# Kernel tuning notes

Hardware: AMD Instinct MI355X
Metric: run time of the kernel (lower is better)

Reference implementation:

```python
import jax, jax.numpy as jnp
import numpy as np

N_NODES = 100000
N_EDGES = 1600000
IN_DIM = 128
HID_DIM = 64
OUT_DIM = 64


def glorot(key, shape):
    lim = np.sqrt(6.0 / (shape[0] + shape[1]))
    return jax.random.uniform(key, shape, jnp.float32, -lim, lim)


def setup_inputs() -> dict:
    key = jax.random.key(0)
    k1, k2, k3, k4 = jax.random.split(key, 4)
    x = jax.random.normal(k1, (N_NODES, IN_DIM), jnp.float32)
    edge_index = jax.random.randint(k2, (2, N_EDGES), 0, N_NODES, jnp.int64)
    W1 = glorot(k3, (IN_DIM, HID_DIM))
    b1 = jnp.zeros((HID_DIM,), jnp.float32)
    W2 = glorot(k4, (HID_DIM, OUT_DIM))
    b2 = jnp.zeros((OUT_DIM,), jnp.float32)
    return {"x": x, "edge_index": edge_index, "W1": W1, "b1": b1, "W2": W2, "b2": b2}


def gcn_conv(x, src, dst, W, b):
    """PyG GCNConv: add self-loops, symmetric D^-1/2 (A+I) D^-1/2 normalization."""
    n = x.shape[0]
    h = x @ W  # [N, F_out] -- transform before propagate (PyG order)
    # degree with self-loops (edge_weight defaults to ones)
    deg = jax.ops.segment_sum(jnp.ones_like(dst, dtype=h.dtype), dst, num_segments=n) + 1.0
    dinv = jax.lax.rsqrt(deg)  # [N]
    norm = dinv[src] * dinv[dst]  # [E]
    msg = h[src] * norm[:, None]  # [E, F_out] gather + scale
    agg = jax.ops.segment_sum(msg, dst, num_segments=n)  # scatter-add
    agg = agg + h * (dinv * dinv)[:, None]  # self-loop contribution
    return agg + b


def reference(x, edge_index, W1, b1, W2, b2):
    src, dst = edge_index[0], edge_index[1]
    h = gcn_conv(x, src, dst, W1, b1)
    h = jax.nn.relu(h)  # dropout is identity in eval mode
    out = gcn_conv(h, src, dst, W2, b2)
    return out
```

## Files before the change

### kernel.cpp

```cpp
#include <hip/hip_runtime.h>


#define FILL_CS 8192
#define BSH 9

__global__ __launch_bounds__(256) void k_hist(const int* __restrict__ dst,
                                              int* __restrict__ hist,
                                              int E, int nbkt) {
  __shared__ int lc[256];
  int c = blockIdx.x;
  lc[threadIdx.x] = 0;
  __syncthreads();
  int base = c * FILL_CS;
  int end = base + FILL_CS;
  if (end > E) end = E;
  for (int e = base + threadIdx.x; e < end; e += 256)
    atomicAdd(&lc[dst[e] >> BSH], 1);
  __syncthreads();
  if (threadIdx.x < nbkt) hist[c * nbkt + threadIdx.x] = lc[threadIdx.x];
}

__global__ __launch_bounds__(256) void k_choff(const int* __restrict__ hist,
                                               int* __restrict__ choff,
                                               int* __restrict__ total,
                                               int nchunk, int nbkt) {
  __shared__ int tmp[256];
  int b = blockIdx.x;
  int c = threadIdx.x;
  int v = (c < nchunk) ? hist[c * nbkt + b] : 0;
  tmp[c] = v;
  __syncthreads();
  for (int off = 1; off < 256; off <<= 1) {
    int t = (c >= off) ? tmp[c - off] : 0;
    __syncthreads();
    tmp[c] += t;
    __syncthreads();
  }
  if (c < nchunk) choff[c * nbkt + b] = tmp[c] - v;
  if (c == 255) total[b] = tmp[255];
}

__global__ __launch_bounds__(256) void k_bbase(const int* __restrict__ total,
                                               int* __restrict__ bbase,
                                               int nbkt, int E) {
  __shared__ int tmp[256];
  int i = threadIdx.x;
  int v = (i < nbkt) ? total[i] : 0;
  tmp[i] = v;
  __syncthreads();
  for (int off = 1; off < 256; off <<= 1) {
    int t = (i >= off) ? tmp[i - off] : 0;
    __syncthreads();
    tmp[i] += t;
    __syncthreads();
  }
  if (i < nbkt) bbase[i] = tmp[i] - v;
  if (i == 0) bbase[nbkt] = E;
}

__global__ __launch_bounds__(256) void k_fill3(const int* __restrict__ src,
                                               const int* __restrict__ dst,
                                               const int* __restrict__ choff,
                                               const int* __restrict__ bbase,
                                               unsigned int* __restrict__ bkt,
                                               int E, int nbkt) {
  __shared__ int cur[256];
  int c = blockIdx.x;
  if (threadIdx.x < nbkt)
    cur[threadIdx.x] = bbase[threadIdx.x] + choff[c * nbkt + threadIdx.x];
  __syncthreads();
  int base = c * FILL_CS;
  int end = base + FILL_CS;
  if (end > E) end = E;
  for (int e = base + threadIdx.x; e < end; e += 256) {
    int d = dst[e];
    int s = src[e];
    int p = atomicAdd(&cur[d >> BSH], 1);
    bkt[p] = ((unsigned int)(d & 511) << 17) | (unsigned int)s;
  }
}

__global__ __launch_bounds__(256) void k_bcount(const unsigned int* __restrict__ bkt,
                                                const int* __restrict__ bbase,
                                                int* __restrict__ cnt, int N) {
  __shared__ int lc[512];
  int b = blockIdx.x;
  lc[threadIdx.x] = 0;
  lc[threadIdx.x + 256] = 0;
  __syncthreads();
  int beg = bbase[b], end = bbase[b + 1];
  for (int i = beg + threadIdx.x; i < end; i += 256)
    atomicAdd(&lc[bkt[i] >> 17], 1);
  __syncthreads();
  int base = b << BSH;
#pragma unroll
  for (int k = 0; k < 2; ++k) {
    int i = threadIdx.x + k * 256;
    if (base + i < N) cnt[base + i] = lc[i];
  }
}

__global__ __launch_bounds__(256) void k_dinv(const int* __restrict__ cnt,
                                              float* __restrict__ dinv, int N) {
  int i = blockIdx.x * 256 + threadIdx.x;
  if (i < N) dinv[i] = rsqrtf((float)cnt[i] + 1.0f);
}

__global__ __launch_bounds__(256) void k_scan1(const int* __restrict__ cnt,
                                               int* __restrict__ row,
                                               int* __restrict__ bsum, int N) {
  __shared__ int tmp[256];
  int i = blockIdx.x * 256 + threadIdx.x;
  int v = (i < N) ? cnt[i] : 0;
  tmp[threadIdx.x] = v;
  __syncthreads();
  for (int off = 1; off < 256; off <<= 1) {
    int t = (threadIdx.x >= off) ? tmp[threadIdx.x - off] : 0;
    __syncthreads();
    tmp[threadIdx.x] += t;
    __syncthreads();
  }
  if (i < N) row[i] = tmp[threadIdx.x] - v;
  if (threadIdx.x == 255) bsum[blockIdx.x] = tmp[255];
}

__global__ __launch_bounds__(512) void k_scan2(int* __restrict__ bsum, int nb) {
  __shared__ int tmp[512];
  int v = (threadIdx.x < nb) ? bsum[threadIdx.x] : 0;
  tmp[threadIdx.x] = v;
  __syncthreads();
  for (int off = 1; off < 512; off <<= 1) {
    int t = (threadIdx.x >= off) ? tmp[threadIdx.x - off] : 0;
    __syncthreads();
    tmp[threadIdx.x] += t;
    __syncthreads();
  }
  if (threadIdx.x < nb) bsum[threadIdx.x] = tmp[threadIdx.x] - v;
}

__global__ __launch_bounds__(256) void k_scan3(int* __restrict__ row,
                                               const int* __restrict__ bsum,
                                               int N, int E) {
  int i = blockIdx.x * 256 + threadIdx.x;
  if (i < N) row[i] += bsum[blockIdx.x];
  if (i == 0) row[N] = E;
}

__global__ __launch_bounds__(256) void k_bfill(const unsigned int* __restrict__ bkt,
                                               const int* __restrict__ bbase,
                                               const int* __restrict__ row,
                                               int* __restrict__ eidx, int N) {
  __shared__ int fl[512];
  int b = blockIdx.x;
  fl[threadIdx.x] = 0;
  fl[threadIdx.x + 256] = 0;
  __syncthreads();
  int beg = bbase[b], end = bbase[b + 1];
  int base = b << BSH;
  for (int i = beg + threadIdx.x; i < end; i += 256) {
    unsigned int v = bkt[i];
    int dl = v >> 17;
    int s = v & 0x1FFFF;
    int ofs = atomicAdd(&fl[dl], 1);
    eidx[row[base + dl] + ofs] = s;
  }
}

template <int K>
__global__ __launch_bounds__(256) void k_gemm(const float* __restrict__ X,
                                              const float* __restrict__ W,
                                              const float* __restrict__ dinv,
                                              float* __restrict__ HS, int N) {
  __shared__ float Xs[64][K + 4];
  __shared__ float Ws[K][64];
  const int t = threadIdx.x;
  const int base = blockIdx.x * 64;

  for (int idx = t * 4; idx < 64 * K; idx += 1024) {
    int r = idx / K, c = idx % K;
    float4 v = make_float4(0.f, 0.f, 0.f, 0.f);
    if (base + r < N)
      v = *reinterpret_cast<const float4*>(X + (size_t)(base + r) * K + c);
    *reinterpret_cast<float4*>(&Xs[r][c]) = v;
  }
  for (int idx = t * 4; idx < K * 64; idx += 1024) {
    float4 v = *reinterpret_cast<const float4*>(W + idx);
    *reinterpret_cast<float4*>(&Ws[0][0] + idx) = v;
  }
  __syncthreads();

  const int n0 = (t >> 4) * 4;
  const int j0 = (t & 15) * 4;
  float acc[4][4];
#pragma unroll
  for (int i = 0; i < 4; ++i)
#pragma unroll
    for (int j = 0; j < 4; ++j) acc[i][j] = 0.f;

  for (int k0 = 0; k0 < K; k0 += 4) {
    float4 xv[4];
#pragma unroll
    for (int i = 0; i < 4; ++i)
      xv[i] = *reinterpret_cast<const float4*>(&Xs[n0 + i][k0]);
#pragma unroll
    for (int kk = 0; kk < 4; ++kk) {
      float4 wv = *reinterpret_cast<const float4*>(&Ws[k0 + kk][j0]);
#pragma unroll
      for (int i = 0; i < 4; ++i) {
        float xs = (kk == 0) ? xv[i].x : (kk == 1) ? xv[i].y
                 : (kk == 2) ? xv[i].z : xv[i].w;
        acc[i][0] = fmaf(xs, wv.x, acc[i][0]);
        acc[i][1] = fmaf(xs, wv.y, acc[i][1]);
        acc[i][2] = fmaf(xs, wv.z, acc[i][2]);
        acc[i][3] = fmaf(xs, wv.w, acc[i][3]);
      }
    }
  }

#pragma unroll
  for (int i = 0; i < 4; ++i) {
    int node = base + n0 + i;
    if (node < N) {
      float di = dinv[node];
      float4 o;
      o.x = acc[i][0] * di; o.y = acc[i][1] * di;
      o.z = acc[i][2] * di; o.w = acc[i][3] * di;
      *reinterpret_cast<float4*>(HS + (size_t)node * 64 + j0) = o;
    }
  }
}

__global__ __launch_bounds__(256) void k_agg(const float* __restrict__ hs,
                                             const int* __restrict__ row,
                                             const int* __restrict__ eidx,
                                             const float* __restrict__ dinv,
                                             const float* __restrict__ bias,
                                             float* __restrict__ out, int N,
                                             int relu) {
  int gid = blockIdx.x * 256 + threadIdx.x;
  int node = gid >> 4;
  if (node >= N) return;
  int q = (gid & 15) * 4;
  int beg = row[node], end = row[node + 1];
  float4 a0 = make_float4(0.f, 0.f, 0.f, 0.f);
  float4 a1 = make_float4(0.f, 0.f, 0.f, 0.f);
  float4 a2 = make_float4(0.f, 0.f, 0.f, 0.f);
  float4 a3 = make_float4(0.f, 0.f, 0.f, 0.f);
  int e = beg;
  for (; e + 3 < end; e += 4) {
    int s0 = eidx[e], s1 = eidx[e + 1], s2 = eidx[e + 2], s3 = eidx[e + 3];
    float4 v0 = *reinterpret_cast<const float4*>(hs + (size_t)s0 * 64 + q);
    float4 v1 = *reinterpret_cast<const float4*>(hs + (size_t)s1 * 64 + q);
    float4 v2 = *reinterpret_cast<const float4*>(hs + (size_t)s2 * 64 + q);
    float4 v3 = *reinterpret_cast<const float4*>(hs + (size_t)s3 * 64 + q);
    a0.x += v0.x; a0.y += v0.y; a0.z += v0.z; a0.w += v0.w;
    a1.x += v1.x; a1.y += v1.y; a1.z += v1.z; a1.w += v1.w;
    a2.x += v2.x; a2.y += v2.y; a2.z += v2.z; a2.w += v2.w;
    a3.x += v3.x; a3.y += v3.y; a3.z += v3.z; a3.w += v3.w;
  }
  for (; e < end; ++e) {
    int s = eidx[e];
    float4 v = *reinterpret_cast<const float4*>(hs + (size_t)s * 64 + q);
    a0.x += v.x; a0.y += v.y; a0.z += v.z; a0.w += v.w;
  }
  float4 self = *reinterpret_cast<const float4*>(hs + (size_t)node * 64 + q);
  float4 bv = *reinterpret_cast<const float4*>(bias + q);
  float dd = dinv[node];
  float4 r;
  r.x = dd * (a0.x + a1.x + a2.x + a3.x + self.x) + bv.x;
  r.y = dd * (a0.y + a1.y + a2.y + a3.y + self.y) + bv.y;
  r.z = dd * (a0.z + a1.z + a2.z + a3.z + self.z) + bv.z;
  r.w = dd * (a0.w + a1.w + a2.w + a3.w + self.w) + bv.w;
  if (relu) {
    r.x = fmaxf(r.x, 0.f); r.y = fmaxf(r.y, 0.f);
    r.z = fmaxf(r.z, 0.f); r.w = fmaxf(r.w, 0.f);
  }
  *reinterpret_cast<float4*>(out + (size_t)node * 64 + q) = r;
}

extern "C" void kernel_launch(void* const* d_in, const int* in_sizes, int n_in,
                              void* d_out, int out_size, void* d_ws, size_t ws_size,
                              hipStream_t stream) {
  const float* x  = (const float*)d_in[0];
  const int*   ei = (const int*)d_in[1];
  const float* W1 = (const float*)d_in[2];
  const float* b1 = (const float*)d_in[3];
  const float* W2 = (const float*)d_in[4];
  const float* b2 = (const float*)d_in[5];
  float* out = (float*)d_out;

  const int N = in_sizes[0] / 128;
  const int E = in_sizes[1] / 2;
  const int* src = ei;
  const int* dstv = ei + E;

  const int nbkt = (N + (1 << BSH) - 1) >> BSH;
  const int nchunk = (E + FILL_CS - 1) / FILL_CS;

  int*   cnt   = (int*)d_ws;
  int*   row   = cnt + 102400;
  float* dinv  = (float*)(cnt + 205056);
  int*   bsum  = cnt + 307456;
  int*   hist  = cnt + 307968;
  int*   choff = cnt + 346624;
  int*   total = cnt + 385280;
  int*   bbase = cnt + 385536;
  unsigned int* bkt = (unsigned int*)(cnt + 385792);
  int*   eidx  = cnt + 1985792;
  float* bufA  = (float*)(cnt + 3585792);

  const int nb = (N + 255) / 256;
  const int ngemm = (N + 63) / 64;
  const int nagg = (N * 16 + 255) / 256;

  k_hist<<<nchunk, 256, 0, stream>>>(dstv, hist, E, nbkt);
  k_choff<<<nbkt, 256, 0, stream>>>(hist, choff, total, nchunk, nbkt);
  k_bbase<<<1, 256, 0, stream>>>(total, bbase, nbkt, E);
  k_fill3<<<nchunk, 256, 0, stream>>>(src, dstv, choff, bbase, bkt, E, nbkt);
  k_bcount<<<nbkt, 256, 0, stream>>>(bkt, bbase, cnt, N);
  k_dinv<<<nb, 256, 0, stream>>>(cnt, dinv, N);
  k_scan1<<<nb, 256, 0, stream>>>(cnt, row, bsum, N);
  k_scan2<<<1, 512, 0, stream>>>(bsum, nb);
  k_scan3<<<nb, 256, 0, stream>>>(row, bsum, N, E);
  k_bfill<<<nbkt, 256, 0, stream>>>(bkt, bbase, row, eidx, N);

  k_gemm<128><<<ngemm, 256, 0, stream>>>(x, W1, dinv, bufA, N);
  k_agg<<<nagg, 256, 0, stream>>>(bufA, row, eidx, dinv, b1, out, N, 1);

  k_gemm<64><<<ngemm, 256, 0, stream>>>(out, W2, dinv, bufA, N);
  k_agg<<<nagg, 256, 0, stream>>>(bufA, row, eidx, dinv, b2, out, N, 0);
}
```

Measured before the change: 361.0 us.

## Fuse bucket count, degree, row scan and CSR fill into one kernel

Replaces six CSR-construction kernels (bucket count, dinv, three-phase global scan, bucket fill) with one per-bucket kernel. Because buckets are already laid out contiguously by bbase, each block computes its row offsets with a local 512-entry shared-memory scan plus the bucket base, so no global scan is needed. The same block writes dinv and fills eidx using shared atomic cursors. This removes five launches and the global round-trips through cnt and row, at the cost of a block-serial scan with more barriers. It also regroups the final accumulator sums in the aggregation kernel.

Measured after the change: 350.7 us. -2.9%, faster.

```diff
diff --git a/kernel.cpp b/kernel.cpp
--- a/kernel.cpp
+++ b/kernel.cpp
@@ -80,89 +80,57 @@
   }
 }
 
-__global__ __launch_bounds__(256) void k_bcount(const unsigned int* __restrict__ bkt,
-                                                const int* __restrict__ bbase,
-                                                int* __restrict__ cnt, int N) {
+__global__ __launch_bounds__(256) void k_bmake(const unsigned int* __restrict__ bkt,
+                                               const int* __restrict__ bbase,
+                                               int* __restrict__ row,
+                                               int* __restrict__ eidx,
+                                               float* __restrict__ dinv,
+                                               int N, int nbkt) {
   __shared__ int lc[512];
+  __shared__ int sc[512];
   int b = blockIdx.x;
-  lc[threadIdx.x] = 0;
-  lc[threadIdx.x + 256] = 0;
+  int t = threadIdx.x;
+  lc[t] = 0; lc[t + 256] = 0;
   __syncthreads();
   int beg = bbase[b], end = bbase[b + 1];
-  for (int i = beg + threadIdx.x; i < end; i += 256)
+  for (int i = beg + t; i < end; i += 256)
     atomicAdd(&lc[bkt[i] >> 17], 1);
   __syncthreads();
+  sc[t] = lc[t]; sc[t + 256] = lc[t + 256];
+  __syncthreads();
+  for (int off = 1; off < 512; off <<= 1) {
+    int v0 = (t >= off) ? sc[t - off] : 0;
+    int v1 = (t + 256 >= off) ? sc[t + 256 - off] : 0;
+    __syncthreads();
+    sc[t] += v0;
+    sc[t + 256] += v1;
+    __syncthreads();
+  }
   int base = b << BSH;
 #pragma unroll
   for (int k = 0; k < 2; ++k) {
-    int i = threadIdx.x + k * 256;
-    if (base + i < N) cnt[base + i] = lc[i];
-  }
-}
-
-__global__ __launch_bounds__(256) void k_dinv(const int* __restrict__ cnt,
-                                              float* __restrict__ dinv, int N) {
-  int i = blockIdx.x * 256 + threadIdx.x;
-  if (i < N) dinv[i] = rsqrtf((float)cnt[i] + 1.0f);
-}
-
-__global__ __launch_bounds__(256) void k_scan1(const int* __restrict__ cnt,
-                                               int* __restrict__ row,
-                                               int* __restrict__ bsum, int N) {
-  __shared__ int tmp[256];
-  int i = blockIdx.x * 256 + threadIdx.x;
-  int v = (i < N) ? cnt[i] : 0;
-  tmp[threadIdx.x] = v;
-  __syncthreads();
-  for (int off = 1; off < 256; off <<= 1) {
-    int t = (threadIdx.x >= off) ? tmp[threadIdx.x - off] : 0;
-    __syncthreads();
-    tmp[threadIdx.x] += t;
-    __syncthreads();
-  }
-  if (i < N) row[i] = tmp[threadIdx.x] - v;
-  if (threadIdx.x == 255) bsum[blockIdx.x] = tmp[255];
-}
-
-__global__ __launch_bounds__(512) void k_scan2(int* __restrict__ bsum, int nb) {
-  __shared__ int tmp[512];
-  int v = (threadIdx.x < nb) ? bsum[threadIdx.x] : 0;
-  tmp[threadIdx.x] = v;
-  __syncthreads();
-  for (int off = 1; off < 512; off <<= 1) {
-    int t = (threadIdx.x >= off) ? tmp[threadIdx.x - off] : 0;
-    __syncthreads();
-    tmp[threadIdx.x] += t;
-    __syncthreads();
-  }
-  if (threadIdx.x < nb) bsum[threadIdx.x] = tmp[threadIdx.x] - v;
-}
-
-__global__ __launch_bounds__(256) void k_scan3(int* __restrict__ row,
-                                               const int* __restrict__ bsum,
-                                               int N, int E) {
-  int i = blockIdx.x * 256 + threadIdx.x;
-  if (i < N) row[i] += bsum[blockIdx.x];
-  if (i == 0) row[N] = E;
-}
-
-__global__ __launch_bounds__(256) void k_bfill(const unsigned int* __restrict__ bkt,
-                                               const int* __restrict__ bbase,
-                                               const int* __restrict__ row,
-                                               int* __restrict__ eidx, int N) {
-  __shared__ int fl[512];
-  int b = blockIdx.x;
-  fl[threadIdx.x] = 0;
-  fl[threadIdx.x + 256] = 0;
-  __syncthreads();
-  int beg = bbase[b], end = bbase[b + 1];
-  int base = b << BSH;
-  for (int i = beg + threadIdx.x; i < end; i += 256) {
+    int i = t + k * 256;
+    int node = base + i;
+    if (node < N) {
+      int excl = sc[i] - lc[i];
+      row[node] = beg + excl;
+      dinv[node] = rsqrtf((float)lc[i] + 1.0f);
+    }
+  }
+  if (b == nbkt - 1 && t == 0) row[N] = end;
+  __syncthreads();
+#pragma unroll
+  for (int k = 0; k < 2; ++k) {
+    int i = t + k * 256;
+    sc[i] = beg + (sc[i] - lc[i]);
+  }
+  __syncthreads();
+  for (int i = beg + t; i < end; i += 256) {
     unsigned int v = bkt[i];
     int dl = v >> 17;
     int s = v & 0x1FFFF;
-    int ofs = atomicAdd(&fl[dl], 1);
-    eidx[row[base + dl] + ofs] = s;
+    int ofs = atomicAdd(&sc[dl], 1);
+    eidx[ofs] = s;
   }
 }
 
@@ -267,10 +235,10 @@
   float4 bv = *reinterpret_cast<const float4*>(bias + q);
   float dd = dinv[node];
   float4 r;
-  r.x = dd * (a0.x + a1.x + a2.x + a3.x + self.x) + bv.x;
-  r.y = dd * (a0.y + a1.y + a2.y + a3.y + self.y) + bv.y;
-  r.z = dd * (a0.z + a1.z + a2.z + a3.z + self.z) + bv.z;
-  r.w = dd * (a0.w + a1.w + a2.w + a3.w + self.w) + bv.w;
+  r.x = dd * ((a0.x + a1.x) + (a2.x + a3.x) + self.x) + bv.x;
+  r.y = dd * ((a0.y + a1.y) + (a2.y + a3.y) + self.y) + bv.y;
+  r.z = dd * ((a0.z + a1.z) + (a2.z + a3.z) + self.z) + bv.z;
+  r.w = dd * ((a0.w + a1.w) + (a2.w + a3.w) + self.w) + bv.w;
   if (relu) {
     r.x = fmaxf(r.x, 0.f); r.y = fmaxf(r.y, 0.f);
     r.z = fmaxf(r.z, 0.f); r.w = fmaxf(r.w, 0.f);
@@ -297,19 +265,16 @@
   const int nbkt = (N + (1 << BSH) - 1) >> BSH;
   const int nchunk = (E + FILL_CS - 1) / FILL_CS;
 
-  int*   cnt   = (int*)d_ws;
-  int*   row   = cnt + 102400;
-  float* dinv  = (float*)(cnt + 205056);
-  int*   bsum  = cnt + 307456;
-  int*   hist  = cnt + 307968;
-  int*   choff = cnt + 346624;
-  int*   total = cnt + 385280;
-  int*   bbase = cnt + 385536;
-  unsigned int* bkt = (unsigned int*)(cnt + 385792);
-  int*   eidx  = cnt + 1985792;
-  float* bufA  = (float*)(cnt + 3585792);
-
-  const int nb = (N + 255) / 256;
+  int*   row   = (int*)d_ws;
+  float* dinv  = (float*)((int*)d_ws + 102400);
+  int*   hist  = (int*)d_ws + 204800;
+  int*   choff = (int*)d_ws + 243216;
+  int*   total = (int*)d_ws + 281632;
+  int*   bbase = (int*)d_ws + 281856;
+  unsigned int* bkt = (unsigned int*)((int*)d_ws + 282112);
+  int*   eidx  = (int*)d_ws + 1882112;
+  float* bufA  = (float*)((int*)d_ws + 3482112);
+
   const int ngemm = (N + 63) / 64;
   const int nagg = (N * 16 + 255) / 256;
 
@@ -317,12 +282,7 @@
   k_choff<<<nbkt, 256, 0, stream>>>(hist, choff, total, nchunk, nbkt);
   k_bbase<<<1, 256, 0, stream>>>(total, bbase, nbkt, E);
   k_fill3<<<nchunk, 256, 0, stream>>>(src, dstv, choff, bbase, bkt, E, nbkt);
-  k_bcount<<<nbkt, 256, 0, stream>>>(bkt, bbase, cnt, N);
-  k_dinv<<<nb, 256, 0, stream>>>(cnt, dinv, N);
-  k_scan1<<<nb, 256, 0, stream>>>(cnt, row, bsum, N);
-  k_scan2<<<1, 512, 0, stream>>>(bsum, nb);
-  k_scan3<<<nb, 256, 0, stream>>>(row, bsum, N, E);
-  k_bfill<<<nbkt, 256, 0, stream>>>(bkt, bbase, row, eidx, N);
+  k_bmake<<<nbkt, 256, 0, stream>>>(bkt, bbase, row, eidx, dinv, N, nbkt);
 
   k_gemm<128><<<ngemm, 256, 0, stream>>>(x, W1, dinv, bufA, N);
   k_agg<<<nagg, 256, 0, stream>>>(bufA, row, eidx, dinv, b1, out, N, 1);
```
